# Kernel tuning notes

Hardware: AMD Instinct MI355X
Metric: run time of the kernel (lower is better)

Reference implementation:

```python
import jax, jax.numpy as jnp
import numpy as np

BETA = 0.25


def setup_inputs() -> dict:
    key = jax.random.key(0)
    k1, k2 = jax.random.split(key)
    x = jax.random.normal(k1, (32, 32, 32, 256), dtype=jnp.float32)
    codebook = jax.random.normal(k2, (1024, 256), dtype=jnp.float32)
    return {"x": x, "codebook": codebook}


def reference(x, codebook):
    D = codebook.shape[1]
    z_fla = x.reshape(-1, D)  # [N, D]
    # squared euclidean distances [N, K]
    dis = (jnp.sum(z_fla ** 2, axis=1, keepdims=True)
           + jnp.sum(codebook ** 2, axis=1)
           - 2.0 * jnp.matmul(z_fla, codebook.T))
    min_encoding_indices = jnp.argmin(dis, axis=1)  # [N] int
    z_q = codebook[min_encoding_indices].reshape(x.shape)
    loss = (jnp.mean((jax.lax.stop_gradient(z_q) - x) ** 2)
            + BETA * jnp.mean((z_q - jax.lax.stop_gradient(x)) ** 2))
    z_q = x + jax.lax.stop_gradient(z_q - x)  # straight-through
    # faithful to source: mean of the index values, then "perplexity" formula
    e_min = jnp.mean(min_encoding_indices.astype(jnp.float32), axis=0)
    perplexity = jnp.exp(-jnp.sum(e_min * jnp.log(e_min + 1e-10)))
    return (loss, z_q, perplexity, min_encoding_indices)
```

## Files before the change

kernel.cpp:

```cpp
#include <hip/hip_runtime.h>
#include <cmath>

#define NROWS 32768
#define DDIM  256
#define KCB   1024

constexpr float TAU = 0.02f;
constexpr int BSTR = 264;

typedef _Float16 half8 __attribute__((ext_vector_type(8)));
typedef float floatx4 __attribute__((ext_vector_type(4)));

__global__ void init_kernel(double* __restrict__ sumsq, int* __restrict__ sumidx) {
  *sumsq = 0.0;
  *sumidx = 0;
}

__global__ __launch_bounds__(64) void prep_kernel(const float* __restrict__ cb,
                                                  float* __restrict__ cn) {
  const int k = blockIdx.x, lane = threadIdx.x;
  float4 v = *(const float4*)(cb + (size_t)k * DDIM + lane * 4);
  double s = (double)v.x * v.x + (double)v.y * v.y
           + (double)v.z * v.z + (double)v.w * v.w;
  #pragma unroll
  for (int off = 32; off; off >>= 1) s += __shfl_down(s, off);
  if (lane == 0) cn[k] = (float)s;
}

__global__ __launch_bounds__(512, 2) void fused_kernel(
    const float* __restrict__ x,
    const float* __restrict__ cb,
    const float* __restrict__ cn,
    float* __restrict__ zq_out,
    float* __restrict__ idx_out,
    double* __restrict__ sumsq,
    int* __restrict__ sumidx) {
  __shared__ __align__(16) _Float16 bs[2][64 * BSTR];
  __shared__ float cn_lds[KCB];
  __shared__ int   bidx[128];
  __shared__ int   bidx2[128];
  __shared__ float m2s[128];
  __shared__ float m3s[128];
  __shared__ __align__(16) float xrow[DDIM];
  __shared__ int   plist[128];
  __shared__ int   flist[128];
  __shared__ int   npair, nfull;
  __shared__ float wred[8];
  __shared__ double rv[8];
  __shared__ int    ri[8];

  const int tid = threadIdx.x;
  const int lane = tid & 63;
  const int w = tid >> 6;
  const int q = lane >> 4;
  const int tx = lane & 15;
  const int row0 = blockIdx.x * 128;

  half8 a_hi[8], a_lo[8];
  {
    const float* xp = x + (size_t)(row0 + w * 16 + tx) * DDIM + q * 8;
    #pragma unroll
    for (int s = 0; s < 8; ++s) {
      float4 v0 = *(const float4*)(xp + s * 32);
      float4 v1 = *(const float4*)(xp + s * 32 + 4);
      half8 h, l;
      _Float16 t;
      t = (_Float16)v0.x; h[0] = t; l[0] = (_Float16)(v0.x - (float)t);
      t = (_Float16)v0.y; h[1] = t; l[1] = (_Float16)(v0.y - (float)t);
      t = (_Float16)v0.z; h[2] = t; l[2] = (_Float16)(v0.z - (float)t);
      t = (_Float16)v0.w; h[3] = t; l[3] = (_Float16)(v0.w - (float)t);
      t = (_Float16)v1.x; h[4] = t; l[4] = (_Float16)(v1.x - (float)t);
      t = (_Float16)v1.y; h[5] = t; l[5] = (_Float16)(v1.y - (float)t);
      t = (_Float16)v1.z; h[6] = t; l[6] = (_Float16)(v1.z - (float)t);
      t = (_Float16)v1.w; h[7] = t; l[7] = (_Float16)(v1.w - (float)t);
      a_hi[s] = h; a_lo[s] = l;
    }
  }
  #pragma unroll
  for (int i = 0; i < 2; ++i) cn_lds[tid + 512 * i] = cn[tid + 512 * i];
  if (tid == 0) { npair = 0; nfull = 0; }

  float4 vld[4];
  auto load_stage = [&](int ct) {
    #pragma unroll
    for (int i = 0; i < 2; ++i) {
      int u = tid + 512 * i;
      const float* p = cb + (size_t)ct * 8192 + (size_t)u * 8;
      vld[2 * i]     = *(const float4*)p;
      vld[2 * i + 1] = *(const float4*)(p + 4);
    }
  };
  auto write_stage = [&](int buf) {
    #pragma unroll
    for (int i = 0; i < 2; ++i) {
      int u = tid + 512 * i;
      int e = u >> 5, c = u & 31;
      float4 v0 = vld[2 * i], v1 = vld[2 * i + 1];
      half8 h, l;
      _Float16 t;
      t = (_Float16)v0.x; h[0] = t; l[0] = (_Float16)(v0.x - (float)t);
      t = (_Float16)v0.y; h[1] = t; l[1] = (_Float16)(v0.y - (float)t);
      t = (_Float16)v0.z; h[2] = t; l[2] = (_Float16)(v0.z - (float)t);
      t = (_Float16)v0.w; h[3] = t; l[3] = (_Float16)(v0.w - (float)t);
      t = (_Float16)v1.x; h[4] = t; l[4] = (_Float16)(v1.x - (float)t);
      t = (_Float16)v1.y; h[5] = t; l[5] = (_Float16)(v1.y - (float)t);
      t = (_Float16)v1.z; h[6] = t; l[6] = (_Float16)(v1.z - (float)t);
      t = (_Float16)v1.w; h[7] = t; l[7] = (_Float16)(v1.w - (float)t);
      *(half8*)&bs[buf][e * BSTR + c * 8] = h;
      *(half8*)&bs[buf][(32 + e) * BSTR + c * 8] = l;
    }
  };

  float v1[4], v2[4], v3[4];
  int i1[4], i2[4];
  #pragma unroll
  for (int r = 0; r < 4; ++r) {
    v1[r] = INFINITY; v2[r] = INFINITY; v3[r] = INFINITY; i1[r] = 0; i2[r] = 0;
  }

  load_stage(0);
  for (int st = 0; st < 32; ++st) {
    const int buf = st & 1;
    write_stage(buf);
    __syncthreads();
    if (st + 1 < 32) load_stage(st + 1);

    floatx4 ahh[2], alh[2], ahl[2];
    #pragma unroll
    for (int ci = 0; ci < 2; ++ci) {
      ahh[ci] = (floatx4){0.f, 0.f, 0.f, 0.f};
      alh[ci] = (floatx4){0.f, 0.f, 0.f, 0.f};
      ahl[ci] = (floatx4){0.f, 0.f, 0.f, 0.f};
    }

    #pragma unroll
    for (int s = 0; s < 8; ++s) {
      #pragma unroll
      for (int ci = 0; ci < 2; ++ci) {
        half8 bh = *(const half8*)&bs[buf][(ci * 16 + tx) * BSTR + (s * 4 + q) * 8];
        half8 bl = *(const half8*)&bs[buf][(32 + ci * 16 + tx) * BSTR + (s * 4 + q) * 8];
        ahh[ci] = __builtin_amdgcn_mfma_f32_16x16x32_f16(a_hi[s], bh, ahh[ci], 0, 0, 0);
        alh[ci] = __builtin_amdgcn_mfma_f32_16x16x32_f16(a_lo[s], bh, alh[ci], 0, 0, 0);
        ahl[ci] = __builtin_amdgcn_mfma_f32_16x16x32_f16(a_hi[s], bl, ahl[ci], 0, 0, 0);
      }
    }

    #pragma unroll
    for (int ci = 0; ci < 2; ++ci) {
      int col = st * 32 + ci * 16 + tx;
      float cnv = cn_lds[col];
      #pragma unroll
      for (int r = 0; r < 4; ++r) {
        float dot = ahh[ci][r] + alh[ci][r] + ahl[ci][r];
        float dist = cnv - 2.f * dot;
        if (dist < v1[r]) {
          v3[r] = v2[r]; v2[r] = v1[r]; i2[r] = i1[r];
          v1[r] = dist; i1[r] = col;
        } else if (dist < v2[r]) {
          v3[r] = v2[r]; v2[r] = dist; i2[r] = col;
        } else if (dist < v3[r]) {
          v3[r] = dist;
        }
      }
    }
  }

  #pragma unroll
  for (int off = 8; off; off >>= 1) {
    #pragma unroll
    for (int r = 0; r < 4; ++r) {
      float ov1 = __shfl_down(v1[r], off, 16);
      int   oi1 = __shfl_down(i1[r], off, 16);
      float ov2 = __shfl_down(v2[r], off, 16);
      int   oi2 = __shfl_down(i2[r], off, 16);
      float ov3 = __shfl_down(v3[r], off, 16);
      bool takeo = (ov1 < v1[r]) || (ov1 == v1[r] && oi1 < i1[r]);
      float n1v = takeo ? ov1 : v1[r];
      int   n1i = takeo ? oi1 : i1[r];
      float l1 = takeo ? v1[r] : v2[r];
      int   l1i = takeo ? i1[r] : i2[r];
      float l2 = takeo ? v2[r] : v3[r];
      float r1 = takeo ? ov2 : ov1;
      int   r1i = takeo ? oi2 : oi1;
      float r2 = takeo ? ov3 : ov2;
      bool t2 = (r1 < l1) || (r1 == l1 && r1i < l1i);
      float n2v = t2 ? r1 : l1;
      int   n2i = t2 ? r1i : l1i;
      float n3v = t2 ? fminf(r2, l1) : fminf(l2, r1);
      v1[r] = n1v; i1[r] = n1i; v2[r] = n2v; i2[r] = n2i; v3[r] = n3v;
    }
  }
  if (tx == 0) {
    #pragma unroll
    for (int r = 0; r < 4; ++r) {
      int R = w * 16 + q * 4 + r;
      bidx[R]  = i1[r];
      bidx2[R] = i2[r];
      m2s[R] = v2[r] - v1[r];
      m3s[R] = v3[r] - v1[r];
    }
  }
  __syncthreads();

  if (tid < 128) {
    if (m3s[tid] < TAU) {
      int p = atomicAdd(&nfull, 1);
      flist[p] = tid;
    } else if (m2s[tid] < TAU) {
      int p = atomicAdd(&npair, 1);
      plist[p] = tid;
    }
  }
  __syncthreads();

  for (int f = 0; f < nfull; ++f) {
    int r = flist[f];
    if (tid < 64) {
      float4 v = *(const float4*)(x + (size_t)(row0 + r) * DDIM + tid * 4);
      xrow[tid * 4 + 0] = v.x; xrow[tid * 4 + 1] = v.y;
      xrow[tid * 4 + 2] = v.z; xrow[tid * 4 + 3] = v.w;
    }
    __syncthreads();
    float4 xv = *(const float4*)&xrow[lane * 4];
    double bestd = 1e300; int bi = 0;
    for (int k = 0; k < 128; ++k) {
      int c = w * 128 + k;
      float4 cv = *(const float4*)(cb + (size_t)c * DDIM + lane * 4);
      double d0 = (double)xv.x - (double)cv.x; double s = d0 * d0;
      double d1 = (double)xv.y - (double)cv.y; s = fma(d1, d1, s);
      double d2 = (double)xv.z - (double)cv.z; s = fma(d2, d2, s);
      double d3 = (double)xv.w - (double)cv.w; s = fma(d3, d3, s);
      #pragma unroll
      for (int off = 32; off; off >>= 1) s += __shfl_down(s, off);
      if (lane == 0 && s < bestd) { bestd = s; bi = c; }
    }
    if (lane == 0) { rv[w] = bestd; ri[w] = bi; }
    __syncthreads();
    if (tid == 0) {
      double bv = rv[0]; int bix = ri[0];
      for (int ww = 1; ww < 8; ++ww)
        if (rv[ww] < bv || (rv[ww] == bv && ri[ww] < bix)) { bv = rv[ww]; bix = ri[ww]; }
      bidx[r] = bix;
    }
    __syncthreads();
  }

  for (int f = w; f < npair; f += 8) {
    int r = plist[f];
    int cA = bidx[r], cB = bidx2[r];
    int c = (lane >= 32) ? cB : cA;
    int ld = lane & 31;
    const float* xp = x  + (size_t)(row0 + r) * DDIM + ld * 8;
    const float* cp = cb + (size_t)c * DDIM + ld * 8;
    double s = 0.0;
    #pragma unroll
    for (int j = 0; j < 8; j += 4) {
      float4 xv = *(const float4*)(xp + j);
      float4 cv = *(const float4*)(cp + j);
      double d0 = (double)xv.x - (double)cv.x; s = fma(d0, d0, s);
      double d1 = (double)xv.y - (double)cv.y; s = fma(d1, d1, s);
      double d2 = (double)xv.z - (double)cv.z; s = fma(d2, d2, s);
      double d3 = (double)xv.w - (double)cv.w; s = fma(d3, d3, s);
    }
    #pragma unroll
    for (int off = 16; off; off >>= 1) s += __shfl_xor(s, off);
    double dA = __shfl(s, 0), dB = __shfl(s, 32);
    if (lane == 0) {
      bool takeB = (dB < dA) || (dB == dA && cB < cA);
      bidx[r] = takeB ? cB : cA;
    }
  }
  __syncthreads();

  if (tid < 128) idx_out[row0 + tid] = (float)bidx[tid];

  float lsum = 0.f;
  #pragma unroll 4
  for (int it = 0; it < 16; ++it) {
    int g = tid + 512 * it;
    int r = g >> 6;
    int c4 = (g & 63) << 2;
    int k = bidx[r] & (KCB - 1);
    float4 cv = *(const float4*)(cb + (size_t)k * DDIM + c4);
    float4 xv = *(const float4*)(x + (size_t)(row0 + r) * DDIM + c4);
    float d0 = cv.x - xv.x, d1 = cv.y - xv.y, d2 = cv.z - xv.z, d3 = cv.w - xv.w;
    lsum = fmaf(d0, d0, lsum); lsum = fmaf(d1, d1, lsum);
    lsum = fmaf(d2, d2, lsum); lsum = fmaf(d3, d3, lsum);
    *(float4*)(zq_out + (size_t)(row0 + r) * DDIM + c4) = cv;
  }
  #pragma unroll
  for (int off = 32; off; off >>= 1) lsum += __shfl_down(lsum, off);
  if (lane == 0) wred[w] = lsum;
  __syncthreads();
  if (tid == 0) {
    double ls = 0.0;
    #pragma unroll
    for (int ww = 0; ww < 8; ++ww) ls += (double)wred[ww];
    atomicAdd(sumsq, ls);
    int si = 0;
    #pragma unroll 8
    for (int r = 0; r < 128; ++r) si += bidx[r] & (KCB - 1);
    atomicAdd(sumidx, si);
  }
}

__global__ void finalize_kernel(const double* __restrict__ sumsq,
                                const int* __restrict__ sumidx,
                                float* __restrict__ out_loss,
                                float* __restrict__ out_perp) {
  double loss = 1.25 * (*sumsq) / 8388608.0;
  double e_min = (double)(*sumidx) / 32768.0;
  double perp = exp(-e_min * log(e_min + 1e-10));
  *out_loss = (float)loss;
  *out_perp = (float)perp;
}

extern "C" void kernel_launch(void* const* d_in, const int* in_sizes, int n_in,
                              void* d_out, int out_size, void* d_ws, size_t ws_size,
                              hipStream_t stream) {
  const float* x  = (const float*)d_in[0];
  const float* cb = (const float*)d_in[1];
  float* out = (float*)d_out;
  float* out_loss = out;
  float* out_zq   = out + 1;
  float* out_perp = out + 1 + 8388608;
  float* out_idx  = out + 2 + 8388608;

  double*   sumsq  = (double*)d_ws;
  int*      sumidx = (int*)((char*)d_ws + 8);
  float*    cn     = (float*)((char*)d_ws + 16);

  hipLaunchKernelGGL(init_kernel, dim3(1), dim3(1), 0, stream, sumsq, sumidx);
  hipLaunchKernelGGL(prep_kernel, dim3(KCB), dim3(64), 0, stream, cb, cn);
  hipLaunchKernelGGL(fused_kernel, dim3(NROWS / 128), dim3(512), 0, stream,
                     x, cb, cn, out_zq, out_idx, sumsq, sumidx);
  hipLaunchKernelGGL(finalize_kernel, dim3(1), dim3(1), 0, stream,
                     sumsq, sumidx, out_loss, out_perp);
}
```

Before: 162.8 us.

## Drop codebook low-half MFMA, fuse norm prep and finalize, widen tiles

Removes the codebook low-precision correction term, so the GEMM uses two fp16 MFMAs (x hi/lo times codebook hi) instead of three. To compensate for the lower accuracy, the exact-recheck threshold TAU is raised. Other changes in the same edit: codebook norms are computed inside the kernel during staging instead of in a separate prep kernel, the codebook tile is widened to 64 entries per stage, the finalize step is folded in using a last-block atomic counter, and the exact fallback search is rewritten to give each thread whole codebook rows. The risk is that the larger TAU sends many more rows to the slow fp64 full-search path.

```diff
diff --git a/kernel.cpp b/kernel.cpp
--- a/kernel.cpp
+++ b/kernel.cpp
@@ -5,36 +5,30 @@
 #define DDIM  256
 #define KCB   1024
 
-constexpr float TAU = 0.02f;
+constexpr float TAU = 0.25f;
 constexpr int BSTR = 264;
 
 typedef _Float16 half8 __attribute__((ext_vector_type(8)));
 typedef float floatx4 __attribute__((ext_vector_type(4)));
 
-__global__ void init_kernel(double* __restrict__ sumsq, int* __restrict__ sumidx) {
+__global__ void init_kernel(double* __restrict__ sumsq,
+                            int* __restrict__ sumidx,
+                            unsigned* __restrict__ done) {
   *sumsq = 0.0;
   *sumidx = 0;
-}
-
-__global__ __launch_bounds__(64) void prep_kernel(const float* __restrict__ cb,
-                                                  float* __restrict__ cn) {
-  const int k = blockIdx.x, lane = threadIdx.x;
-  float4 v = *(const float4*)(cb + (size_t)k * DDIM + lane * 4);
-  double s = (double)v.x * v.x + (double)v.y * v.y
-           + (double)v.z * v.z + (double)v.w * v.w;
-  #pragma unroll
-  for (int off = 32; off; off >>= 1) s += __shfl_down(s, off);
-  if (lane == 0) cn[k] = (float)s;
+  *done = 0u;
 }
 
 __global__ __launch_bounds__(512, 2) void fused_kernel(
     const float* __restrict__ x,
     const float* __restrict__ cb,
-    const float* __restrict__ cn,
     float* __restrict__ zq_out,
     float* __restrict__ idx_out,
+    float* __restrict__ out_loss,
+    float* __restrict__ out_perp,
     double* __restrict__ sumsq,
-    int* __restrict__ sumidx) {
+    int* __restrict__ sumidx,
+    unsigned* __restrict__ done) {
   __shared__ __align__(16) _Float16 bs[2][64 * BSTR];
   __shared__ float cn_lds[KCB];
   __shared__ int   bidx[128];
@@ -76,38 +70,37 @@
       a_hi[s] = h; a_lo[s] = l;
     }
   }
-  #pragma unroll
-  for (int i = 0; i < 2; ++i) cn_lds[tid + 512 * i] = cn[tid + 512 * i];
   if (tid == 0) { npair = 0; nfull = 0; }
 
-  float4 vld[4];
+  float4 vld[8];
   auto load_stage = [&](int ct) {
     #pragma unroll
-    for (int i = 0; i < 2; ++i) {
-      int u = tid + 512 * i;
-      const float* p = cb + (size_t)ct * 8192 + (size_t)u * 8;
-      vld[2 * i]     = *(const float4*)p;
-      vld[2 * i + 1] = *(const float4*)(p + 4);
+    for (int i = 0; i < 4; ++i) {
+      int p = tid + 512 * i;
+      const float* src = cb + (size_t)ct * 16384 + (size_t)p * 8;
+      vld[2 * i]     = *(const float4*)src;
+      vld[2 * i + 1] = *(const float4*)(src + 4);
     }
   };
-  auto write_stage = [&](int buf) {
-    #pragma unroll
-    for (int i = 0; i < 2; ++i) {
-      int u = tid + 512 * i;
-      int e = u >> 5, c = u & 31;
+  auto write_stage = [&](int buf, int ct) {
+    #pragma unroll
+    for (int i = 0; i < 4; ++i) {
+      int p = tid + 512 * i;
+      int e = p >> 5, c = p & 31;
       float4 v0 = vld[2 * i], v1 = vld[2 * i + 1];
-      half8 h, l;
-      _Float16 t;
-      t = (_Float16)v0.x; h[0] = t; l[0] = (_Float16)(v0.x - (float)t);
-      t = (_Float16)v0.y; h[1] = t; l[1] = (_Float16)(v0.y - (float)t);
-      t = (_Float16)v0.z; h[2] = t; l[2] = (_Float16)(v0.z - (float)t);
-      t = (_Float16)v0.w; h[3] = t; l[3] = (_Float16)(v0.w - (float)t);
-      t = (_Float16)v1.x; h[4] = t; l[4] = (_Float16)(v1.x - (float)t);
-      t = (_Float16)v1.y; h[5] = t; l[5] = (_Float16)(v1.y - (float)t);
-      t = (_Float16)v1.z; h[6] = t; l[6] = (_Float16)(v1.z - (float)t);
-      t = (_Float16)v1.w; h[7] = t; l[7] = (_Float16)(v1.w - (float)t);
+      half8 h;
+      h[0] = (_Float16)v0.x; h[1] = (_Float16)v0.y;
+      h[2] = (_Float16)v0.z; h[3] = (_Float16)v0.w;
+      h[4] = (_Float16)v1.x; h[5] = (_Float16)v1.y;
+      h[6] = (_Float16)v1.z; h[7] = (_Float16)v1.w;
       *(half8*)&bs[buf][e * BSTR + c * 8] = h;
-      *(half8*)&bs[buf][(32 + e) * BSTR + c * 8] = l;
+      double s = (double)v0.x * v0.x + (double)v0.y * v0.y
+               + (double)v0.z * v0.z + (double)v0.w * v0.w
+               + (double)v1.x * v1.x + (double)v1.y * v1.y
+               + (double)v1.z * v1.z + (double)v1.w * v1.w;
+      #pragma unroll
+      for (int off = 16; off; off >>= 1) s += __shfl_down(s, off, 32);
+      if ((tid & 31) == 0) cn_lds[ct * 64 + e] = (float)s;
     }
   };
 
@@ -119,39 +112,36 @@
   }
 
   load_stage(0);
-  for (int st = 0; st < 32; ++st) {
+  for (int st = 0; st < 16; ++st) {
     const int buf = st & 1;
-    write_stage(buf);
+    write_stage(buf, st);
     __syncthreads();
-    if (st + 1 < 32) load_stage(st + 1);
-
-    floatx4 ahh[2], alh[2], ahl[2];
-    #pragma unroll
-    for (int ci = 0; ci < 2; ++ci) {
+    if (st + 1 < 16) load_stage(st + 1);
+
+    floatx4 ahh[4], alh[4];
+    #pragma unroll
+    for (int ci = 0; ci < 4; ++ci) {
       ahh[ci] = (floatx4){0.f, 0.f, 0.f, 0.f};
       alh[ci] = (floatx4){0.f, 0.f, 0.f, 0.f};
-      ahl[ci] = (floatx4){0.f, 0.f, 0.f, 0.f};
     }
 
     #pragma unroll
     for (int s = 0; s < 8; ++s) {
       #pragma unroll
-      for (int ci = 0; ci < 2; ++ci) {
+      for (int ci = 0; ci < 4; ++ci) {
         half8 bh = *(const half8*)&bs[buf][(ci * 16 + tx) * BSTR + (s * 4 + q) * 8];
-        half8 bl = *(const half8*)&bs[buf][(32 + ci * 16 + tx) * BSTR + (s * 4 + q) * 8];
         ahh[ci] = __builtin_amdgcn_mfma_f32_16x16x32_f16(a_hi[s], bh, ahh[ci], 0, 0, 0);
         alh[ci] = __builtin_amdgcn_mfma_f32_16x16x32_f16(a_lo[s], bh, alh[ci], 0, 0, 0);
-        ahl[ci] = __builtin_amdgcn_mfma_f32_16x16x32_f16(a_hi[s], bl, ahl[ci], 0, 0, 0);
       }
     }
 
     #pragma unroll
-    for (int ci = 0; ci < 2; ++ci) {
-      int col = st * 32 + ci * 16 + tx;
+    for (int ci = 0; ci < 4; ++ci) {
+      int col = st * 64 + ci * 16 + tx;
       float cnv = cn_lds[col];
       #pragma unroll
       for (int r = 0; r < 4; ++r) {
-        float dot = ahh[ci][r] + alh[ci][r] + ahl[ci][r];
+        float dot = ahh[ci][r] + alh[ci][r];
         float dist = cnv - 2.f * dot;
         if (dist < v1[r]) {
           v3[r] = v2[r]; v2[r] = v1[r]; i2[r] = i1[r];
@@ -221,20 +211,30 @@
       xrow[tid * 4 + 2] = v.z; xrow[tid * 4 + 3] = v.w;
     }
     __syncthreads();
-    float4 xv = *(const float4*)&xrow[lane * 4];
-    double bestd = 1e300; int bi = 0;
-    for (int k = 0; k < 128; ++k) {
-      int c = w * 128 + k;
-      float4 cv = *(const float4*)(cb + (size_t)c * DDIM + lane * 4);
-      double d0 = (double)xv.x - (double)cv.x; double s = d0 * d0;
-      double d1 = (double)xv.y - (double)cv.y; s = fma(d1, d1, s);
-      double d2 = (double)xv.z - (double)cv.z; s = fma(d2, d2, s);
-      double d3 = (double)xv.w - (double)cv.w; s = fma(d3, d3, s);
-      #pragma unroll
-      for (int off = 32; off; off >>= 1) s += __shfl_down(s, off);
-      if (lane == 0 && s < bestd) { bestd = s; bi = c; }
-    }
-    if (lane == 0) { rv[w] = bestd; ri[w] = bi; }
+    double bd = 1e300; int bi = 0;
+    #pragma unroll
+    for (int j = 0; j < 2; ++j) {
+      int c = 2 * tid + j;
+      const float* cp = cb + (size_t)c * DDIM;
+      double s0 = 0.0, s1 = 0.0, s2 = 0.0, s3 = 0.0;
+      for (int d = 0; d < DDIM; d += 4) {
+        float4 cv = *(const float4*)(cp + d);
+        float4 xv = *(const float4*)&xrow[d];
+        double d0 = (double)xv.x - (double)cv.x; s0 = fma(d0, d0, s0);
+        double d1 = (double)xv.y - (double)cv.y; s1 = fma(d1, d1, s1);
+        double d2 = (double)xv.z - (double)cv.z; s2 = fma(d2, d2, s2);
+        double d3 = (double)xv.w - (double)cv.w; s3 = fma(d3, d3, s3);
+      }
+      double s = (s0 + s1) + (s2 + s3);
+      if (s < bd) { bd = s; bi = c; }
+    }
+    #pragma unroll
+    for (int off = 32; off; off >>= 1) {
+      double ov = __shfl_down(bd, off);
+      int oi = __shfl_down(bi, off);
+      if (ov < bd || (ov == bd && oi < bi)) { bd = ov; bi = oi; }
+    }
+    if (lane == 0) { rv[w] = bd; ri[w] = bi; }
     __syncthreads();
     if (tid == 0) {
       double bv = rv[0]; int bix = ri[0];
@@ -301,18 +301,20 @@
     #pragma unroll 8
     for (int r = 0; r < 128; ++r) si += bidx[r] & (KCB - 1);
     atomicAdd(sumidx, si);
-  }
-}
-
-__global__ void finalize_kernel(const double* __restrict__ sumsq,
-                                const int* __restrict__ sumidx,
-                                float* __restrict__ out_loss,
-                                float* __restrict__ out_perp) {
-  double loss = 1.25 * (*sumsq) / 8388608.0;
-  double e_min = (double)(*sumidx) / 32768.0;
-  double perp = exp(-e_min * log(e_min + 1e-10));
-  *out_loss = (float)loss;
-  *out_perp = (float)perp;
+
+    __threadfence();
+    unsigned prev = atomicAdd(done, 1u);
+    if (prev == gridDim.x - 1) {
+      __threadfence();
+      double ss = atomicAdd(sumsq, 0.0);
+      int    sidx = atomicAdd(sumidx, 0);
+      double loss = 1.25 * ss / 8388608.0;
+      double e_min = (double)sidx / 32768.0;
+      double perp = exp(-e_min * log(e_min + 1e-10));
+      *out_loss = (float)loss;
+      *out_perp = (float)perp;
+    }
+  }
 }
 
 extern "C" void kernel_launch(void* const* d_in, const int* in_sizes, int n_in,
@@ -328,12 +330,11 @@
 
   double*   sumsq  = (double*)d_ws;
   int*      sumidx = (int*)((char*)d_ws + 8);
-  float*    cn     = (float*)((char*)d_ws + 16);
-
-  hipLaunchKernelGGL(init_kernel, dim3(1), dim3(1), 0, stream, sumsq, sumidx);
-  hipLaunchKernelGGL(prep_kernel, dim3(KCB), dim3(64), 0, stream, cb, cn);
+  unsigned* done   = (unsigned*)((char*)d_ws + 12);
+
+  hipLaunchKernelGGL(init_kernel, dim3(1), dim3(1), 0, stream,
+                     sumsq, sumidx, done);
   hipLaunchKernelGGL(fused_kernel, dim3(NROWS / 128), dim3(512), 0, stream,
-                     x, cb, cn, out_zq, out_idx, sumsq, sumidx);
-  hipLaunchKernelGGL(finalize_kernel, dim3(1), dim3(1), 0, stream,
-                     sumsq, sumidx, out_loss, out_perp);
+                     x, cb, out_zq, out_idx, out_loss, out_perp,
+                     sumsq, sumidx, done);
 }
```

After: 191.6 us. +17.7%, slower.
